# Performance work log

Hardware: AMD Instinct MI355X
Metric: run time of the kernel (lower is better)

## Reference

```python
import jax, jax.numpy as jnp
import numpy as np

NP_, NA_ = 50000, 20000
D_IN, D_HID, D_OUT = 128, 128, 64
E_W, E_C, E_R = 250000, 500000, 250000


def setup_inputs() -> dict:
    key = jax.random.key(0)
    ks = jax.random.split(key, 14)
    s_in = 1.0 / np.sqrt(D_IN)
    s_h = 1.0 / np.sqrt(D_HID)
    return {
        "x_paper": jax.random.normal(ks[0], (NP_, D_IN), jnp.float32),
        "x_author": jax.random.normal(ks[1], (NA_, D_IN), jnp.float32),
        "Wl1": jax.random.normal(ks[2], (3, D_HID, D_IN), jnp.float32) * s_in,
        "bl1": jax.random.normal(ks[3], (3, D_HID), jnp.float32) * 0.01,
        "Wr1": jax.random.normal(ks[4], (3, D_HID, D_IN), jnp.float32) * s_in,
        "Wl2": jax.random.normal(ks[5], (3, D_OUT, D_HID), jnp.float32) * s_h,
        "bl2": jax.random.normal(ks[6], (3, D_OUT), jnp.float32) * 0.01,
        "Wr2": jax.random.normal(ks[7], (3, D_OUT, D_HID), jnp.float32) * s_h,
        "writes_src": jax.random.randint(ks[8], (E_W,), 0, NA_),
        "writes_dst": jax.random.randint(ks[9], (E_W,), 0, NP_),
        "cites_src": jax.random.randint(ks[10], (E_C,), 0, NP_),
        "cites_dst": jax.random.randint(ks[11], (E_C,), 0, NP_),
        "rev_src": jax.random.randint(ks[12], (E_R,), 0, NP_),
        "rev_dst": jax.random.randint(ks[13], (E_R,), 0, NA_),
    }


def _sage(x_src, x_dst, src, dst, Wl, bl, Wr, n_dst):
    # PyG SAGEConv(aggr='mean'): lin_l(mean_j x_src[j]) + lin_r(x_dst)
    agg = jax.ops.segment_sum(x_src[src], dst, num_segments=n_dst)
    cnt = jax.ops.segment_sum(jnp.ones_like(dst, dtype=x_src.dtype), dst,
                              num_segments=n_dst)
    agg = agg / jnp.maximum(cnt, 1.0)[:, None]  # degree-0 nodes -> 0 (PyG scatter-mean)
    return agg @ Wl.T + bl + x_dst @ Wr.T


def reference(x_paper, x_author, Wl1, bl1, Wr1, Wl2, bl2, Wr2,
              writes_src, writes_dst, cites_src, cites_dst, rev_src, rev_dst):
    def hetero_layer(xp, xa, Wl, bl, Wr):
        # HeteroConv(aggr='mean'): average per-relation outputs per dst node type
        op = 0.5 * (_sage(xa, xp, writes_src, writes_dst, Wl[0], bl[0], Wr[0], NP_)
                    + _sage(xp, xp, cites_src, cites_dst, Wl[1], bl[1], Wr[1], NP_))
        oa = _sage(xp, xa, rev_src, rev_dst, Wl[2], bl[2], Wr[2], NA_)
        return op, oa

    hp, ha = hetero_layer(x_paper, x_author, Wl1, bl1, Wr1)
    hp, ha = jax.nn.relu(hp), jax.nn.relu(ha)  # norm_type='none', dropout eval-mode
    hp, _ = hetero_layer(hp, ha, Wl2, bl2, Wr2)
    return hp  # logits for category='paper', [NP_, D_OUT]
```

## Files before the change

### kernel.cpp

```cpp
#include <hip/hip_runtime.h>

#define NP 50000
#define NA 20000
#define E_W 250000
#define E_C 500000
#define E_R 250000
#define E_TOT (E_W + E_C + E_R)
#define CAP 48
#define RBLK 4096
#define NSEG 245
#define PNODES 15000
#define CHK 500
#define NCH 30
#define NBIN 240

typedef __attribute__((ext_vector_type(8))) short short8;
typedef __attribute__((ext_vector_type(4))) float floatx4;
typedef __attribute__((ext_vector_type(2))) float floatx2;

__device__ __forceinline__ unsigned short f2bf(float f) {
    unsigned u = __float_as_uint(f);
    return (unsigned short)((u + 0x7FFFu + ((u >> 16) & 1u)) >> 16);
}
__device__ __forceinline__ float bflo(unsigned v) { return __uint_as_float(v << 16); }
__device__ __forceinline__ float bfhi(unsigned v) { return __uint_as_float(v & 0xFFFF0000u); }

__device__ __forceinline__ int node_idx(int node) {
    if (node < 2 * NP) {
        int rel1 = node >= NP;
        int d = node - (rel1 ? NP : 0);
        int p2 = d / 6250;
        return p2 * PNODES + (d - p2 * 6250) + (rel1 ? 6250 : 0);
    }
    int d = node - 2 * NP;
    int p2 = d / 2500;
    return p2 * PNODES + 12500 + (d - p2 * 2500);
}

__device__ __forceinline__ int frag_off(int NT, int j, int n, int k) {
    int t = n >> 4, ln = n & 15;
    int kb = k >> 5, q = (k >> 3) & 3, r = k & 7;
    return (((j * NT + t) * 4 + kb) * 64 + q * 16 + ln) * 8 + r;
}

__device__ __forceinline__ void prep_body(
    int idx,
    const float* __restrict__ xp, const float* __restrict__ xa,
    const float* __restrict__ Wl1, const float* __restrict__ Wr1,
    const float* __restrict__ Wl2, const float* __restrict__ Wr2,
    const float* __restrict__ bl1, const float* __restrict__ bl2,
    unsigned short* __restrict__ xpb, unsigned short* __restrict__ xab,
    unsigned* __restrict__ xp8, unsigned* __restrict__ xa8,
    unsigned short* __restrict__ Wp1, unsigned short* __restrict__ Wa1,
    unsigned short* __restrict__ Wt2, unsigned short* __restrict__ Wr2s,
    float* __restrict__ bias_p1, float* __restrict__ bias_a1,
    float* __restrict__ bias_p2) {
    const int n4p = NP * 32, n4a = NA * 32;
    if (idx < n4p + n4a) {
        const float* s; unsigned short* d; unsigned* d8; int i = idx;
        if (i < n4p) { s = xp; d = xpb; d8 = xp8; }
        else { s = xa; d = xab; d8 = xa8; i -= n4p; }
        float4 v = ((const float4*)s)[i];
        ushort4 u;
        u.x = f2bf(v.x); u.y = f2bf(v.y); u.z = f2bf(v.z); u.w = f2bf(v.w);
        ((ushort4*)d)[i] = u;
        int w = __builtin_amdgcn_cvt_pk_fp8_f32(v.x, v.y, 0, false);
        w = __builtin_amdgcn_cvt_pk_fp8_f32(v.z, v.w, w, true);
        d8[i] = (unsigned)w;
        return;
    }
    int j = idx - (n4p + n4a);
    if (j < 49152) {
        int jj = j >> 14, rem = j & 16383, n = rem >> 7, k = rem & 127;
        float v = (jj == 0)   ? 0.5f * Wl1[rem]
                  : (jj == 1) ? 0.5f * Wl1[16384 + rem]
                              : 0.5f * (Wr1[rem] + Wr1[16384 + rem]);
        Wp1[frag_off(8, jj, n, k)] = f2bf(v);
    } else if (j < 81920) {
        int i2 = j - 49152;
        int jj = i2 >> 14, rem = i2 & 16383, n = rem >> 7, k = rem & 127;
        float v = (jj == 0) ? Wl1[2 * 16384 + rem] : Wr1[2 * 16384 + rem];
        Wa1[frag_off(8, jj, n, k)] = f2bf(v);
    } else if (j < 98304) {
        int i2 = j - 81920;
        int jj = i2 >> 13, rem = i2 & 8191, n = rem >> 7, k = rem & 127;
        float v = 0.5f * Wl2[jj * 8192 + rem];
        Wt2[frag_off(4, jj, n, k)] = f2bf(v);
    } else if (j < 106496) {
        int i2 = j - 98304;
        int n = i2 >> 7, k = i2 & 127;
        float v = 0.5f * (Wr2[i2] + Wr2[8192 + i2]);
        Wr2s[frag_off(4, 0, n, k)] = f2bf(v);
    } else if (j < 106496 + 320) {
        int b = j - 106496;
        if (b < 128) bias_p1[b] = 0.5f * (bl1[b] + bl1[128 + b]);
        else if (b < 256) bias_a1[b - 128] = bl1[256 + b - 128];
        else bias_p2[b - 256] = 0.5f * (bl2[b - 256] + bl2[64 + b - 256]);
    }
}

__device__ __forceinline__ void edge_bin(
    int e, const int* __restrict__ w_src, const int* __restrict__ w_dst,
    const int* __restrict__ c_src, const int* __restrict__ c_dst,
    const int* __restrict__ r_src, const int* __restrict__ r_dst,
    int& bin, int& sub, int& src) {
    bool isC = (e >= E_W) & (e < E_W + E_C);
    bool isR = e >= E_W + E_C;
    const int* db = isR ? r_dst : (isC ? c_dst : w_dst);
    const int* sb = isR ? r_src : (isC ? c_src : w_src);
    int idx = e - (isC ? E_W : 0) - (isR ? (E_W + E_C) : 0);
    int d = db[idx];
    src = sb[idx];
    int p, local;
    if (isR) { p = d / 2500; local = 12500 + d - p * 2500; }
    else { p = d / 6250; local = (d - p * 6250) + (isC ? 6250 : 0); }
    int ch = local / CHK;
    bin = p * NCH + ch;
    sub = local - ch * CHK;
}

__device__ __forceinline__ void route_body(
    int bid, const int* __restrict__ w_src, const int* __restrict__ w_dst,
    const int* __restrict__ c_src, const int* __restrict__ c_dst,
    const int* __restrict__ r_src, const int* __restrict__ r_dst,
    unsigned* __restrict__ seg, int* __restrict__ segoff, int* __restrict__ segcnt,
    int* cnt_s, int* base_s, int* cur_s) {
    int tid = threadIdx.x, lane = tid & 63;
    for (int k = tid; k < NBIN; k += 256) cnt_s[k] = 0;
    __syncthreads();
#pragma unroll 4
    for (int u = 0; u < 16; ++u) {
        int e = bid * RBLK + u * 256 + tid;
        if (e < E_TOT) {
            int bin, sub, src;
            edge_bin(e, w_src, w_dst, c_src, c_dst, r_src, r_dst, bin, sub, src);
            atomicAdd(&cnt_s[bin], 1);
        }
    }
    __syncthreads();
    if (tid < 64) {
        int v[4], tot = 0;
#pragma unroll
        for (int q = 0; q < 4; ++q) {
            int k = tid * 4 + q;
            v[q] = (k < NBIN) ? cnt_s[k] : 0;
            tot += v[q];
        }
        int sc = tot;
#pragma unroll
        for (int ofs = 1; ofs < 64; ofs <<= 1) {
            int t = __shfl_up(sc, ofs, 64);
            if (lane >= ofs) sc += t;
        }
        int run = sc - tot;
#pragma unroll
        for (int q = 0; q < 4; ++q) {
            int k = tid * 4 + q;
            if (k < NBIN) { base_s[k] = run; run += v[q]; }
        }
    }
    __syncthreads();
    for (int k = tid; k < NBIN; k += 256) {
        segoff[bid * NBIN + k] = base_s[k];
        segcnt[bid * NBIN + k] = cnt_s[k];
        cur_s[k] = base_s[k];
    }
    __syncthreads();
    unsigned* segb = seg + (size_t)bid * RBLK;
#pragma unroll 4
    for (int u = 0; u < 16; ++u) {
        int e = bid * RBLK + u * 256 + tid;
        if (e < E_TOT) {
            int bin, sub, src;
            edge_bin(e, w_src, w_dst, c_src, c_dst, r_src, r_dst, bin, sub, src);
            int pos = atomicAdd(&cur_s[bin], 1);
            segb[pos] = (unsigned)src | ((unsigned)sub << 16);
        }
    }
}

__global__ __launch_bounds__(256) void route_prep(
    const float* xp, const float* xa, const float* Wl1, const float* Wr1,
    const float* Wl2, const float* Wr2, const float* bl1, const float* bl2,
    unsigned short* xpb, unsigned short* xab, unsigned* xp8, unsigned* xa8,
    unsigned short* Wp1, unsigned short* Wa1, unsigned short* Wt2, unsigned short* Wr2s,
    float* bias_p1, float* bias_a1, float* bias_p2,
    const int* w_src, const int* w_dst, const int* c_src, const int* c_dst,
    const int* r_src, const int* r_dst,
    unsigned* seg, int* segoff, int* segcnt) {
    __shared__ int cnt_s[NBIN], base_s[NBIN], cur_s[NBIN];
    if ((int)blockIdx.x < NSEG)
        route_body(blockIdx.x, w_src, w_dst, c_src, c_dst, r_src, r_dst,
                   seg, segoff, segcnt, cnt_s, base_s, cur_s);
    else
        prep_body((blockIdx.x - NSEG) * 256 + threadIdx.x, xp, xa, Wl1, Wr1, Wl2, Wr2,
                  bl1, bl2, xpb, xab, xp8, xa8, Wp1, Wa1, Wt2, Wr2s,
                  bias_p1, bias_a1, bias_p2);
}

__global__ __launch_bounds__(256) void fill2c(
    const unsigned* __restrict__ seg, const int* __restrict__ segoff,
    const int* __restrict__ segcnt, int* __restrict__ cnt,
    unsigned short* __restrict__ csr) {
    __shared__ unsigned short rows[CHK * CAP];
    __shared__ int cursor[CHK];
    __shared__ int offs[NSEG], cnts[NSEG];
    int k = blockIdx.x, tid = threadIdx.x;
    for (int s = tid; s < NSEG; s += 256) {
        offs[s] = segoff[s * NBIN + k];
        cnts[s] = segcnt[s * NBIN + k];
    }
    for (int l = tid; l < CHK; l += 256) cursor[l] = 0;
    __syncthreads();
    int grp = tid >> 4, gl = tid & 15;
    for (int s = grp; s < NSEG; s += 16) {
        int n = cnts[s];
        const unsigned* sp = seg + (size_t)s * RBLK + offs[s];
        for (int i = gl; i < n; i += 16) {
            unsigned v = sp[i];
            int sub = v >> 16, src = v & 0xFFFFu;
            int pos = atomicAdd(&cursor[sub], 1);
            if (pos < CAP) rows[sub * CAP + pos] = (unsigned short)src;
        }
    }
    __syncthreads();
    int p = k / NCH, ch = k - p * NCH;
    int gbase = p * PNODES + ch * CHK;
    for (int l = tid; l < CHK; l += 256) cnt[gbase + l] = cursor[l];
    const unsigned* rU = (const unsigned*)rows;
    unsigned* cU = (unsigned*)csr + (size_t)gbase * (CAP / 2);
    for (int i = tid; i < CHK * (CAP / 2); i += 256) cU[i] = rU[i];
}

__global__ void agg_pad(const unsigned* __restrict__ s0, unsigned short* __restrict__ d0,
                        const unsigned* __restrict__ s1, unsigned short* __restrict__ d1,
                        const unsigned* __restrict__ s2, unsigned short* __restrict__ d2,
                        const int* __restrict__ cnt, const unsigned short* __restrict__ csr) {
    int g = blockIdx.x * 8 + (threadIdx.x >> 5);
    int lane = threadIdx.x & 63;
    int sl = lane & 31, hw = lane & 32;
    const unsigned* sp; unsigned short* dst; int node, dummy;
    if (g < NP) { sp = s0; dst = d0; node = g; dummy = NA; }
    else if (g < 2 * NP) { sp = s1; dst = d1; node = g - NP; dummy = NP; }
    else if (g < 2 * NP + NA) { sp = s2; dst = d2; node = g - 2 * NP; dummy = NP; }
    else return;
    int idx = node_idx(g);
    int deg = cnt[idx];
    int degc = deg < CAP ? deg : CAP;
    const unsigned short* row = csr + (size_t)idx * CAP;
    int ei0 = (sl < degc) ? (int)row[sl] : dummy;
    int ei1 = (32 + sl < degc) ? (int)row[32 + sl] : dummy;
    int degw = degc;
    int other = __shfl_xor(degw, 32, 64);
    if (other > degw) degw = other;
    float a0 = 0.f, a1 = 0.f, a2 = 0.f, a3 = 0.f;
    float b0 = 0.f, b1 = 0.f, b2 = 0.f, b3 = 0.f;
    for (int i = 0; i < degw; i += 8) {
        unsigned v[8];
#pragma unroll
        for (int u = 0; u < 8; ++u) {
            int ii = i + u;
            int esrc = (ii < 32) ? ei0 : ei1;
            int qq = __shfl(esrc, hw | (ii & 31), 64);
            qq = (ii < degc) ? qq : dummy;
            v[u] = sp[(size_t)qq * 32 + sl];
        }
#pragma unroll
        for (int u = 0; u < 8; ++u) {
            floatx2 lo = __builtin_amdgcn_cvt_pk_f32_fp8(v[u], false);
            floatx2 hi = __builtin_amdgcn_cvt_pk_f32_fp8(v[u], true);
            if (u & 1) { b0 += lo.x; b1 += lo.y; b2 += hi.x; b3 += hi.y; }
            else       { a0 += lo.x; a1 += lo.y; a2 += hi.x; a3 += hi.y; }
        }
    }
    float scl = deg > 0 ? 1.f / (float)deg : 0.f;
    float r0 = (a0 + b0) * scl, r1 = (a1 + b1) * scl;
    float r2 = (a2 + b2) * scl, r3 = (a3 + b3) * scl;
    unsigned wlo = ((unsigned)f2bf(r1) << 16) | (unsigned)f2bf(r0);
    unsigned whi = ((unsigned)f2bf(r3) << 16) | (unsigned)f2bf(r2);
    ((uint2*)dst)[(size_t)node * 32 + sl] = make_uint2(wlo, whi);
}

__global__ void agg2(const unsigned short* __restrict__ ta, const unsigned short* __restrict__ tp,
                     const int* __restrict__ cnt, const unsigned short* __restrict__ csr,
                     const float* __restrict__ sp_in, const float* __restrict__ bias_p2,
                     float* __restrict__ out) {
    int node = blockIdx.x * 8 + (threadIdx.x >> 5);
    if (node >= NP) return;
    int lane = threadIdx.x & 63;
    int sl = lane & 31;
    int hw = lane & 32;
    int p2 = node / 6250;
    int base = p2 * PNODES + (node - p2 * 6250);
    float r0 = 0.f, r1 = 0.f;
#pragma unroll
    for (int rel = 0; rel < 2; ++rel) {
        int dummy = (rel == 0) ? NA : NP;
        const unsigned* sp = (const unsigned*)((rel == 0) ? ta : tp);
        int idx = base + (rel ? 6250 : 0);
        int deg = cnt[idx];
        int degc = deg < CAP ? deg : CAP;
        const unsigned short* row = csr + (size_t)idx * CAP;
        int ei0 = (sl < degc) ? (int)row[sl] : dummy;
        int ei1 = (32 + sl < degc) ? (int)row[32 + sl] : dummy;
        int degw = degc;
        int other = __shfl_xor(degw, 32, 64);
        if (other > degw) degw = other;
        float s0 = 0.f, s1 = 0.f, t0 = 0.f, t1 = 0.f;
        for (int i = 0; i < degw; i += 8) {
            unsigned v[8];
#pragma unroll
            for (int u = 0; u < 8; ++u) {
                int ii = i + u;
                int esrc = (ii < 32) ? ei0 : ei1;
                int qq = __shfl(esrc, hw | (ii & 31), 64);
                qq = (ii < degc) ? qq : dummy;
                v[u] = sp[(size_t)qq * 32 + sl];
            }
#pragma unroll
            for (int u = 0; u < 8; ++u) {
                if (u & 1) { t0 += bflo(v[u]); t1 += bfhi(v[u]); }
                else       { s0 += bflo(v[u]); s1 += bfhi(v[u]); }
            }
        }
        float scl = deg > 0 ? 1.f / (float)deg : 0.f;
        r0 += (s0 + t0) * scl; r1 += (s1 + t1) * scl;
    }
    float2 spv = ((const float2*)sp_in)[(size_t)node * 32 + sl];
    float2 bv = ((const float2*)bias_p2)[sl];
    ((float2*)out)[(size_t)node * 32 + sl] =
        make_float2(r0 + spv.x + bv.x, r1 + spv.y + bv.y);
}

template <int J, bool SP>
__device__ __forceinline__ void l1_core(
    const unsigned short* __restrict__ A0, const unsigned short* __restrict__ A1,
    const unsigned short* __restrict__ A2, const unsigned short* __restrict__ Wf,
    const float* __restrict__ bias,
    const unsigned short* __restrict__ Wt, unsigned short* __restrict__ tout,
    const unsigned short* __restrict__ Wsp, float* __restrict__ spout,
    unsigned short (*hT)[136], int M, int blk) {
    int tid = threadIdx.x;
    int wave = tid >> 6, lane = tid & 63;
    int ln = lane & 15, quad = lane >> 4;
    int row = blk * 64 + wave * 16 + ln;
    int rowc = row < M ? row : M - 1;
    const unsigned short* As[3] = {A0, A1, A2};
    floatx4 acc[8];
#pragma unroll
    for (int t = 0; t < 8; ++t) acc[t] = (floatx4){0.f, 0.f, 0.f, 0.f};
#pragma unroll
    for (int j = 0; j < J; ++j) {
        const unsigned short* A = As[j] + (long)rowc * 128 + quad * 8;
        const unsigned short* Wj = Wf + j * (128 * 128) + lane * 8;
#pragma unroll
        for (int kb = 0; kb < 4; ++kb) {
            short8 af = *(const short8*)(A + kb * 32);
#pragma unroll
            for (int t = 0; t < 8; ++t) {
                short8 bf = *(const short8*)(Wj + (t * 4 + kb) * 512);
                acc[t] = __builtin_amdgcn_mfma_f32_16x16x32_bf16(af, bf, acc[t], 0, 0, 0);
            }
        }
    }
    int orow0 = blk * 64 + wave * 16 + quad * 4;
    int lrow0 = wave * 16 + quad * 4;
#pragma unroll
    for (int t = 0; t < 8; ++t) {
        int col = t * 16 + ln;
        float bv = bias[col];
#pragma unroll
        for (int r = 0; r < 4; ++r) {
            float v = fmaxf(acc[t][r] + bv, 0.f);
            hT[lrow0 + r][col] = f2bf(v);
        }
    }
    __syncthreads();
    floatx4 tacc[4], sacc[4];
#pragma unroll
    for (int t = 0; t < 4; ++t) {
        tacc[t] = (floatx4){0.f, 0.f, 0.f, 0.f};
        sacc[t] = (floatx4){0.f, 0.f, 0.f, 0.f};
    }
#pragma unroll
    for (int kb = 0; kb < 4; ++kb) {
        short8 af = *(const short8*)&hT[wave * 16 + ln][quad * 8 + kb * 32];
#pragma unroll
        for (int t = 0; t < 4; ++t) {
            short8 bf = *(const short8*)(Wt + (t * 4 + kb) * 512 + lane * 8);
            tacc[t] = __builtin_amdgcn_mfma_f32_16x16x32_bf16(af, bf, tacc[t], 0, 0, 0);
            if (SP) {
                short8 bs = *(const short8*)(Wsp + (t * 4 + kb) * 512 + lane * 8);
                sacc[t] = __builtin_amdgcn_mfma_f32_16x16x32_bf16(af, bs, sacc[t], 0, 0, 0);
            }
        }
    }
#pragma unroll
    for (int t = 0; t < 4; ++t) {
        int col = t * 16 + ln;
#pragma unroll
        for (int r = 0; r < 4; ++r) {
            int orow = orow0 + r;
            if (orow < M) {
                tout[(long)orow * 64 + col] = f2bf(tacc[t][r]);
                if (SP) spout[(long)orow * 64 + col] = sacc[t][r];
            }
        }
    }
}

__global__ __launch_bounds__(256) void gemm_l1f(
    const unsigned short* aggP1, const unsigned short* aggP2, const unsigned short* xpb,
    const unsigned short* Wp1, const float* bias_p1,
    const unsigned short* aggA, const unsigned short* xab,
    const unsigned short* Wa1, const float* bias_a1,
    const unsigned short* Wt2, const unsigned short* Wr2s,
    unsigned short* ta, unsigned short* tp, float* sp) {
    __shared__ unsigned short hT[64][136];
    constexpr int PB = (NP + 63) / 64;
    if ((int)blockIdx.x < PB)
        l1_core<3, true>(aggP1, aggP2, xpb, Wp1, bias_p1, Wt2 + 64 * 128, tp, Wr2s, sp,
                         hT, NP, blockIdx.x);
    else
        l1_core<2, false>(aggA, xab, nullptr, Wa1, bias_a1, Wt2, ta, nullptr, nullptr,
                          hT, NA, blockIdx.x - PB);
}

extern "C" void kernel_launch(void* const* d_in, const int* in_sizes, int n_in,
                              void* d_out, int out_size, void* d_ws, size_t ws_size,
                              hipStream_t stream) {
    (void)in_sizes; (void)n_in; (void)out_size; (void)ws_size;
    const float* xp  = (const float*)d_in[0];
    const float* xa  = (const float*)d_in[1];
    const float* Wl1 = (const float*)d_in[2];
    const float* bl1 = (const float*)d_in[3];
    const float* Wr1 = (const float*)d_in[4];
    const float* Wl2 = (const float*)d_in[5];
    const float* bl2 = (const float*)d_in[6];
    const float* Wr2 = (const float*)d_in[7];
    const int* w_src = (const int*)d_in[8];
    const int* w_dst = (const int*)d_in[9];
    const int* c_src = (const int*)d_in[10];
    const int* c_dst = (const int*)d_in[11];
    const int* r_src = (const int*)d_in[12];
    const int* r_dst = (const int*)d_in[13];
    float* out = (float*)d_out;

    char* p = (char*)d_ws;
    auto alloc = [&](size_t bytes) {
        char* r = p;
        p += (bytes + 255) & ~(size_t)255;
        return r;
    };
    unsigned short* xpb   = (unsigned short*)alloc((size_t)NP * 128 * 2);
    unsigned short* xab   = (unsigned short*)alloc((size_t)NA * 128 * 2);
    unsigned*       xp8   = (unsigned*)alloc((size_t)(NP + 1) * 128);
    unsigned*       xa8   = (unsigned*)alloc((size_t)(NA + 1) * 128);
    unsigned short* aggP1 = (unsigned short*)alloc((size_t)NP * 128 * 2);
    unsigned short* aggP2 = (unsigned short*)alloc((size_t)NP * 128 * 2);
    unsigned short* aggA  = (unsigned short*)alloc((size_t)NA * 128 * 2);
    unsigned short* ta    = (unsigned short*)alloc((size_t)(NA + 1) * 64 * 2);
    unsigned short* tp    = (unsigned short*)alloc((size_t)(NP + 1) * 64 * 2);
    float*          sp    = (float*)alloc((size_t)NP * 64 * 4);
    int*            cnt    = (int*)alloc((size_t)8 * PNODES * 4);
    unsigned short* csr    = (unsigned short*)alloc((size_t)8 * PNODES * CAP * 2);
    unsigned*       seg    = (unsigned*)alloc((size_t)NSEG * RBLK * 4);
    int*            segoff = (int*)alloc((size_t)NSEG * NBIN * 4);
    int*            segcnt = (int*)alloc((size_t)NSEG * NBIN * 4);
    unsigned short* Wp1  = (unsigned short*)alloc(3 * 128 * 128 * 2);
    unsigned short* Wa1  = (unsigned short*)alloc(2 * 128 * 128 * 2);
    unsigned short* Wt2  = (unsigned short*)alloc(2 * 64 * 128 * 2);
    unsigned short* Wr2s = (unsigned short*)alloc(64 * 128 * 2);
    float* bias_p1 = (float*)alloc(128 * 4);
    float* bias_a1 = (float*)alloc(128 * 4);
    float* bias_p2 = (float*)alloc(64 * 4);

    hipMemsetAsync(xp8 + (size_t)NP * 32, 0, 128, stream);
    hipMemsetAsync(xa8 + (size_t)NA * 32, 0, 128, stream);
    hipMemsetAsync(ta + (size_t)NA * 64, 0, 128, stream);
    hipMemsetAsync(tp + (size_t)NP * 64, 0, 128, stream);

    int prep_threads = (NP + NA) * 32 + 106496 + 320;
    int prep_blocks = (prep_threads + 255) / 256;
    route_prep<<<NSEG + prep_blocks, 256, 0, stream>>>(
        xp, xa, Wl1, Wr1, Wl2, Wr2, bl1, bl2,
        xpb, xab, xp8, xa8, Wp1, Wa1, Wt2, Wr2s, bias_p1, bias_a1, bias_p2,
        w_src, w_dst, c_src, c_dst, r_src, r_dst, seg, segoff, segcnt);

    fill2c<<<NBIN, 256, 0, stream>>>(seg, segoff, segcnt, cnt, csr);

    agg_pad<<<(2 * NP + NA + 7) / 8, 256, 0, stream>>>(xa8, aggP1, xp8, aggP2, xp8, aggA,
                                                       cnt, csr);

    gemm_l1f<<<(NP + 63) / 64 + (NA + 63) / 64, 256, 0, stream>>>(
        aggP1, aggP2, xpb, Wp1, bias_p1, aggA, xab, Wa1, bias_a1, Wt2, Wr2s, ta, tp, sp);

    agg2<<<(NP + 7) / 8, 256, 0, stream>>>(ta, tp, cnt, csr, sp, bias_p2, out);
}
```

Baseline: 223.0 us.

## Fuse CSR fill with first-layer mean aggregation using shared-memory rows

Merges the CSR-building kernel and the layer-1 neighbor aggregation into one kernel. The aggregation now reads neighbor indices straight from the shared-memory rows just built, instead of rereading csr/cnt from global memory in a separate launch. Bins are halved (CHK 250, 480 bins) and blocks grow to 512 threads, with author-relation chunks scheduled first. Author-relation CSR rows are no longer written to global memory since layer 2 does not need them. The risk is fewer, heavier blocks doing the gather work, which lowers parallelism compared with the old many-block gather kernel.

```diff
diff --git a/kernel.cpp b/kernel.cpp
--- a/kernel.cpp
+++ b/kernel.cpp
@@ -10,9 +10,9 @@
 #define RBLK 4096
 #define NSEG 245
 #define PNODES 15000
-#define CHK 500
-#define NCH 30
-#define NBIN 240
+#define CHK 250
+#define NCH 60
+#define NBIN 480
 
 typedef __attribute__((ext_vector_type(8))) short short8;
 typedef __attribute__((ext_vector_type(4))) float floatx4;
@@ -24,18 +24,6 @@
 }
 __device__ __forceinline__ float bflo(unsigned v) { return __uint_as_float(v << 16); }
 __device__ __forceinline__ float bfhi(unsigned v) { return __uint_as_float(v & 0xFFFF0000u); }
-
-__device__ __forceinline__ int node_idx(int node) {
-    if (node < 2 * NP) {
-        int rel1 = node >= NP;
-        int d = node - (rel1 ? NP : 0);
-        int p2 = d / 6250;
-        return p2 * PNODES + (d - p2 * 6250) + (rel1 ? 6250 : 0);
-    }
-    int d = node - 2 * NP;
-    int p2 = d / 2500;
-    return p2 * PNODES + 12500 + (d - p2 * 2500);
-}
 
 __device__ __forceinline__ int frag_off(int NT, int j, int n, int k) {
     int t = n >> 4, ln = n & 15;
@@ -139,10 +127,10 @@
     }
     __syncthreads();
     if (tid < 64) {
-        int v[4], tot = 0;
-#pragma unroll
-        for (int q = 0; q < 4; ++q) {
-            int k = tid * 4 + q;
+        int v[8], tot = 0;
+#pragma unroll
+        for (int q = 0; q < 8; ++q) {
+            int k = tid * 8 + q;
             v[q] = (k < NBIN) ? cnt_s[k] : 0;
             tot += v[q];
         }
@@ -154,8 +142,8 @@
         }
         int run = sc - tot;
 #pragma unroll
-        for (int q = 0; q < 4; ++q) {
-            int k = tid * 4 + q;
+        for (int q = 0; q < 8; ++q) {
+            int k = tid * 8 + q;
             if (k < NBIN) { base_s[k] = run; run += v[q]; }
         }
     }
@@ -198,22 +186,30 @@
                   bias_p1, bias_a1, bias_p2);
 }
 
-__global__ __launch_bounds__(256) void fill2c(
+__global__ __launch_bounds__(512) void fill_agg(
     const unsigned* __restrict__ seg, const int* __restrict__ segoff,
     const int* __restrict__ segcnt, int* __restrict__ cnt,
-    unsigned short* __restrict__ csr) {
-    __shared__ unsigned short rows[CHK * CAP];
+    unsigned short* __restrict__ csr,
+    const unsigned* __restrict__ xp8, const unsigned* __restrict__ xa8,
+    unsigned short* __restrict__ aggP1, unsigned short* __restrict__ aggP2,
+    unsigned short* __restrict__ aggA) {
+    __shared__ __align__(16) unsigned short rows[CHK * CAP];
     __shared__ int cursor[CHK];
     __shared__ int offs[NSEG], cnts[NSEG];
-    int k = blockIdx.x, tid = threadIdx.x;
-    for (int s = tid; s < NSEG; s += 256) {
+    int tid = threadIdx.x;
+    int b = blockIdx.x, p, ch;
+    if (b < 80)       { p = b / 10; ch = 50 + b % 10; }
+    else if (b < 280) { int t = b - 80;  p = t / 25; ch = 25 + t % 25; }
+    else              { int t = b - 280; p = t / 25; ch = t % 25; }
+    int k = p * NCH + ch;
+    for (int s = tid; s < NSEG; s += 512) {
         offs[s] = segoff[s * NBIN + k];
         cnts[s] = segcnt[s * NBIN + k];
     }
-    for (int l = tid; l < CHK; l += 256) cursor[l] = 0;
+    for (int l = tid; l < CHK; l += 512) cursor[l] = 0;
     __syncthreads();
     int grp = tid >> 4, gl = tid & 15;
-    for (int s = grp; s < NSEG; s += 16) {
+    for (int s = grp; s < NSEG; s += 32) {
         int n = cnts[s];
         const unsigned* sp = seg + (size_t)s * RBLK + offs[s];
         for (int i = gl; i < n; i += 16) {
@@ -224,61 +220,47 @@
         }
     }
     __syncthreads();
-    int p = k / NCH, ch = k - p * NCH;
-    int gbase = p * PNODES + ch * CHK;
-    for (int l = tid; l < CHK; l += 256) cnt[gbase + l] = cursor[l];
-    const unsigned* rU = (const unsigned*)rows;
-    unsigned* cU = (unsigned*)csr + (size_t)gbase * (CAP / 2);
-    for (int i = tid; i < CHK * (CAP / 2); i += 256) cU[i] = rU[i];
-}
-
-__global__ void agg_pad(const unsigned* __restrict__ s0, unsigned short* __restrict__ d0,
-                        const unsigned* __restrict__ s1, unsigned short* __restrict__ d1,
-                        const unsigned* __restrict__ s2, unsigned short* __restrict__ d2,
-                        const int* __restrict__ cnt, const unsigned short* __restrict__ csr) {
-    int g = blockIdx.x * 8 + (threadIdx.x >> 5);
-    int lane = threadIdx.x & 63;
-    int sl = lane & 31, hw = lane & 32;
-    const unsigned* sp; unsigned short* dst; int node, dummy;
-    if (g < NP) { sp = s0; dst = d0; node = g; dummy = NA; }
-    else if (g < 2 * NP) { sp = s1; dst = d1; node = g - NP; dummy = NP; }
-    else if (g < 2 * NP + NA) { sp = s2; dst = d2; node = g - 2 * NP; dummy = NP; }
-    else return;
-    int idx = node_idx(g);
-    int deg = cnt[idx];
-    int degc = deg < CAP ? deg : CAP;
-    const unsigned short* row = csr + (size_t)idx * CAP;
-    int ei0 = (sl < degc) ? (int)row[sl] : dummy;
-    int ei1 = (32 + sl < degc) ? (int)row[32 + sl] : dummy;
-    int degw = degc;
-    int other = __shfl_xor(degw, 32, 64);
-    if (other > degw) degw = other;
-    float a0 = 0.f, a1 = 0.f, a2 = 0.f, a3 = 0.f;
-    float b0 = 0.f, b1 = 0.f, b2 = 0.f, b3 = 0.f;
-    for (int i = 0; i < degw; i += 8) {
-        unsigned v[8];
-#pragma unroll
-        for (int u = 0; u < 8; ++u) {
-            int ii = i + u;
-            int esrc = (ii < 32) ? ei0 : ei1;
-            int qq = __shfl(esrc, hw | (ii & 31), 64);
-            qq = (ii < degc) ? qq : dummy;
-            v[u] = sp[(size_t)qq * 32 + sl];
-        }
-#pragma unroll
-        for (int u = 0; u < 8; ++u) {
-            floatx2 lo = __builtin_amdgcn_cvt_pk_f32_fp8(v[u], false);
-            floatx2 hi = __builtin_amdgcn_cvt_pk_f32_fp8(v[u], true);
-            if (u & 1) { b0 += lo.x; b1 += lo.y; b2 += hi.x; b3 += hi.y; }
-            else       { a0 += lo.x; a1 += lo.y; a2 += hi.x; a3 += hi.y; }
-        }
-    }
-    float scl = deg > 0 ? 1.f / (float)deg : 0.f;
-    float r0 = (a0 + b0) * scl, r1 = (a1 + b1) * scl;
-    float r2 = (a2 + b2) * scl, r3 = (a3 + b3) * scl;
-    unsigned wlo = ((unsigned)f2bf(r1) << 16) | (unsigned)f2bf(r0);
-    unsigned whi = ((unsigned)f2bf(r3) << 16) | (unsigned)f2bf(r2);
-    ((uint2*)dst)[(size_t)node * 32 + sl] = make_uint2(wlo, whi);
+    if (ch < 50) {
+        int gbase = p * PNODES + ch * CHK;
+        for (int l = tid; l < CHK; l += 512) cnt[gbase + l] = cursor[l];
+        const unsigned* rU = (const unsigned*)rows;
+        unsigned* cU = (unsigned*)csr + (size_t)gbase * (CAP / 2);
+        for (int i = tid; i < CHK * (CAP / 2); i += 512) cU[i] = rU[i];
+    }
+    const unsigned* src8; unsigned short* dst; int nodebase, dummy;
+    if (ch < 25)      { src8 = xa8; dst = aggP1; nodebase = p * 6250 + ch * CHK;        dummy = NA; }
+    else if (ch < 50) { src8 = xp8; dst = aggP2; nodebase = p * 6250 + (ch - 25) * CHK; dummy = NP; }
+    else              { src8 = xp8; dst = aggA;  nodebase = p * 2500 + (ch - 50) * CHK; dummy = NP; }
+    int g = tid >> 5, sl = tid & 31;
+    for (int l = g; l < CHK; l += 16) {
+        int deg = cursor[l];
+        int degc = deg < CAP ? deg : CAP;
+        float a0 = 0.f, a1 = 0.f, a2 = 0.f, a3 = 0.f;
+        float b0 = 0.f, b1 = 0.f, b2 = 0.f, b3 = 0.f;
+        for (int i = 0; i < degc; i += 8) {
+            short8 rr = *(const short8*)&rows[l * CAP + i];
+            unsigned v[8];
+#pragma unroll
+            for (int u = 0; u < 8; ++u) {
+                int ii = i + u;
+                int q = (ii < degc) ? (int)(unsigned short)rr[u] : dummy;
+                v[u] = src8[(size_t)q * 32 + sl];
+            }
+#pragma unroll
+            for (int u = 0; u < 8; ++u) {
+                floatx2 lo = __builtin_amdgcn_cvt_pk_f32_fp8(v[u], false);
+                floatx2 hi = __builtin_amdgcn_cvt_pk_f32_fp8(v[u], true);
+                if (u & 1) { b0 += lo.x; b1 += lo.y; b2 += hi.x; b3 += hi.y; }
+                else       { a0 += lo.x; a1 += lo.y; a2 += hi.x; a3 += hi.y; }
+            }
+        }
+        float scl = deg > 0 ? 1.f / (float)deg : 0.f;
+        float r0 = (a0 + b0) * scl, r1 = (a1 + b1) * scl;
+        float r2 = (a2 + b2) * scl, r3 = (a3 + b3) * scl;
+        unsigned wlo = ((unsigned)f2bf(r1) << 16) | (unsigned)f2bf(r0);
+        unsigned whi = ((unsigned)f2bf(r3) << 16) | (unsigned)f2bf(r2);
+        ((uint2*)dst)[(size_t)(nodebase + l) * 32 + sl] = make_uint2(wlo, whi);
+    }
 }
 
 __global__ void agg2(const unsigned short* __restrict__ ta, const unsigned short* __restrict__ tp,
@@ -487,10 +469,8 @@
         xpb, xab, xp8, xa8, Wp1, Wa1, Wt2, Wr2s, bias_p1, bias_a1, bias_p2,
         w_src, w_dst, c_src, c_dst, r_src, r_dst, seg, segoff, segcnt);
 
-    fill2c<<<NBIN, 256, 0, stream>>>(seg, segoff, segcnt, cnt, csr);
-
-    agg_pad<<<(2 * NP + NA + 7) / 8, 256, 0, stream>>>(xa8, aggP1, xp8, aggP2, xp8, aggA,
-                                                       cnt, csr);
+    fill_agg<<<NBIN, 512, 0, stream>>>(seg, segoff, segcnt, cnt, csr,
+                                       xp8, xa8, aggP1, aggP2, aggA);
 
     gemm_l1f<<<(NP + 63) / 64 + (NA + 63) / 64, 256, 0, stream>>>(
         aggP1, aggP2, xpb, Wp1, bias_p1, aggA, xab, Wa1, bias_a1, Wt2, Wr2s, ta, tp, sp);
```

Measured after the change: 214.0 us. 4.0% less time.
